# Performance work log

Measured on AMD Instinct MI355X. Metric: run time of the kernel, lower is better.

## Reference

```python
import jax, jax.numpy as jnp
import numpy as np

BN_EPS = 1e-5
LEAKY_SLOPE = 0.2


def setup_inputs() -> dict:
    key = jax.random.key(0)
    k1, k2 = jax.random.split(key, 2)
    B, C, N, O, K = 8, 64, 4096, 64, 20
    x = jax.random.normal(k1, (B, C, N), dtype=jnp.float32)
    W = jax.random.normal(k2, (O, 2 * C), dtype=jnp.float32) * 0.05  # 1x1 conv weight
    gamma = jnp.ones((O,), dtype=jnp.float32)
    beta = jnp.zeros((O,), dtype=jnp.float32)
    return {"x": x, "W": W, "gamma": gamma, "beta": beta, "k": K}


def reference(x, W, gamma, beta, k):
    # x: (B, C, N)
    xt = jnp.transpose(x, (0, 2, 1))  # (B, N, C)
    # kNN via squared euclidean distances (same ordering as cdist p=2)
    sq = jnp.sum(xt * xt, axis=-1)  # (B, N)
    d2 = sq[:, :, None] + sq[:, None, :] - 2.0 * jnp.einsum('bnc,bmc->bnm', xt, xt)
    idx = jax.lax.top_k(-d2, k)[1]  # (B, N, k) nearest neighbors (incl. self)
    # gather neighbor features: (B, N, k, C)
    xj = jax.vmap(lambda f, i: f[i])(xt, idx)
    xi = xt[:, :, None, :]  # (B, N, 1, C)
    edge = jnp.concatenate([xj - xi, jnp.broadcast_to(xi, xj.shape)], axis=-1)  # (B, N, k, 2C)
    # 1x1 conv == channel GEMM
    h = jnp.einsum('bnkc,oc->bnko', edge, W)  # (B, N, k, O)
    # BatchNorm2d, training-mode batch statistics over (B, N, k) per channel
    mean = jnp.mean(h, axis=(0, 1, 2))
    var = jnp.mean(jnp.square(h - mean), axis=(0, 1, 2))
    hn = (h - mean) * jax.lax.rsqrt(var + BN_EPS) * gamma + beta
    # LeakyReLU(0.2); dropout omitted (eval / identity)
    act = jnp.where(hn >= 0, hn, LEAKY_SLOPE * hn)
    # max over the k neighbors -> (B, N, O) -> (B, O, N)
    out = jnp.max(act, axis=2)
    return jnp.transpose(out, (0, 2, 1))
```

## Files before the change

kernel.cpp:

```cpp
#include <hip/hip_runtime.h>
#include <math.h>

#define Bn 8
#define Cc 64
#define Nn 4096
#define Oo 64
#define Kk 20
#define Kh 10
#define QCAP 24
#define NTOT (Bn*Nn*Kk)

typedef __attribute__((ext_vector_type(8))) short short8;
typedef __attribute__((ext_vector_type(4))) float f32x4;

__device__ __forceinline__ unsigned bf16_rn(float v) {
  unsigned u = __float_as_uint(v);
  return (u + 0x7FFFu + ((u >> 16) & 1)) >> 16;
}

__device__ __forceinline__ float pair_swap_f(float v) {
  return __int_as_float(__builtin_amdgcn_mov_dpp(__float_as_int(v), 0xB1, 0xF, 0xF, true));
}
__device__ __forceinline__ int pair_swap_i(int v) {
  return __builtin_amdgcn_mov_dpp(v, 0xB1, 0xF, 0xF, true);
}

__global__ __launch_bounds__(256) void k_split(const float* __restrict__ x,
                                               unsigned short* __restrict__ xs3,
                                               float* __restrict__ sqv) {
  __shared__ float xs[64][68];
  int tid = threadIdx.x;
  int b = blockIdx.x & 7;
  int n0 = (blockIdx.x >> 3) << 6;
  for (int i = 0; i < 4; i++) {
    int c = i * 16 + (tid >> 4);
    int n = (tid & 15) * 4;
    float4 v = *(const float4*)&x[((size_t)b * Cc + c) * Nn + n0 + n];
    *(float4*)&xs[c][n] = v;
  }
  __syncthreads();
  for (int i = 0; i < 4; i++) {
    int n = i * 16 + (tid >> 4);
    int c = (tid & 15) * 4;
    ushort4 h4, m4, l4;
    unsigned short* hp = (unsigned short*)&h4;
    unsigned short* mp = (unsigned short*)&m4;
    unsigned short* lp = (unsigned short*)&l4;
#pragma unroll
    for (int j = 0; j < 4; j++) {
      float v = xs[c + j][n];
      unsigned hb = bf16_rn(v);
      float hf = __uint_as_float(hb << 16);
      float r1 = v - hf;
      unsigned mb = bf16_rn(r1);
      float mf = __uint_as_float(mb << 16);
      float r2 = r1 - mf;
      unsigned lb = bf16_rn(r2);
      hp[j] = (unsigned short)hb;
      mp[j] = (unsigned short)mb;
      lp[j] = (unsigned short)lb;
    }
    size_t o = ((size_t)(b << 12) + n0 + n) * 192 + c;
    *(ushort4*)&xs3[o] = h4;
    *(ushort4*)&xs3[o + 64] = m4;
    *(ushort4*)&xs3[o + 128] = l4;
  }
  if (tid < 64) {
    float s = 0.f;
#pragma unroll
    for (int c = 0; c < 64; c++) { float v = xs[c][tid]; s = fmaf(v, v, s); }
    sqv[b * Nn + n0 + tid] = s;
  }
}

__global__ __launch_bounds__(256) void k_y1z(const float* __restrict__ x,
                                             const float* __restrict__ Wm,
                                             float* __restrict__ y1,
                                             float* __restrict__ z) {
  __shared__ float xs[64][68];
  __shared__ float Wl[64][129];
  int tid = threadIdx.x;
  int b = blockIdx.x & 7;
  int n0 = (blockIdx.x >> 3) << 6;
  for (int i = tid; i < 64 * 128; i += 256) Wl[i >> 7][i & 127] = Wm[i];
  for (int i = 0; i < 4; i++) {
    int c = i * 16 + (tid >> 4);
    int n = (tid & 15) * 4;
    float4 v = *(const float4*)&x[((size_t)b * Cc + c) * Nn + n0 + n];
    *(float4*)&xs[c][n] = v;
  }
  __syncthreads();
  int o = tid & 63, ng = tid >> 6;
  for (int p = 0; p < 4; p++) {
    int nb = p * 16 + ng * 4;
    float a1[4] = {0.f, 0.f, 0.f, 0.f};
    float a2[4] = {0.f, 0.f, 0.f, 0.f};
#pragma unroll 8
    for (int c = 0; c < 64; c++) {
      float4 xv = *(const float4*)&xs[c][nb];
      float w1v = Wl[o][c], w2v = Wl[o][64 + c];
      float xa[4] = {xv.x, xv.y, xv.z, xv.w};
#pragma unroll
      for (int j = 0; j < 4; j++) {
        a1[j] = fmaf(xa[j], w1v, a1[j]);
        a2[j] = fmaf(xa[j], w2v, a2[j]);
      }
    }
#pragma unroll
    for (int j = 0; j < 4; j++) {
      size_t off = ((size_t)b * Nn + n0 + nb + j) * 64 + o;
      y1[off] = a1[j];
      z[off] = a2[j] - a1[j];
    }
  }
}

__global__ __launch_bounds__(512, 4) void k_knn(const unsigned short* __restrict__ xs3,
                                                const float* __restrict__ sqv,
                                                int* __restrict__ idxout) {
  __shared__ alignas(16) short Bs[2][12288];
  __shared__ float thrS[2][64];
  __shared__ float sqs[2][64];
  __shared__ alignas(16) float qk[2][64][QCAP];
  __shared__ alignas(16) unsigned short qm[2][64][QCAP];
  __shared__ int qcnt[2][64];

  const int tid = threadIdx.x;
  const int lane = tid & 63;
  const int w = tid >> 6;
  const int grp = w >> 2;
  const int wg = w & 3;
  const int tig = tid & 255;
  const int b = blockIdx.x & 7;
  const int n0 = (blockIdx.x >> 3) << 6;
  const int lm = lane & 15;
  const int q = lane >> 4;
  const bool handler = (lane < 32);
  const int hrow = wg * 16 + (lane >> 1);
  const bool isL = (lane & 1) == 0;
  const int rowq = wg * 16 + q * 4;

  const unsigned long long fullseg = 0xFFFFull << (q * 16);
  const unsigned long long window = ((1ull << lane) - 1) & fullseg;

  float hk[Kh];
  int hix[Kh];
#pragma unroll
  for (int kk = 0; kk < Kh; kk++) { hk[kk] = INFINITY; hix[kk] = 0; }

  if (handler && !isL) { thrS[grp][hrow] = INFINITY; qcnt[grp][hrow] = 0; }

  const size_t arow = ((size_t)(b << 12) + n0 + wg * 16 + lm) * 192;
  short8 ah0 = *(const short8*)&xs3[arow + q * 8];
  short8 ah1 = *(const short8*)&xs3[arow + 32 + q * 8];
  short8 am0 = *(const short8*)&xs3[arow + 64 + q * 8];
  short8 am1 = *(const short8*)&xs3[arow + 96 + q * 8];
  short8 al0 = *(const short8*)&xs3[arow + 128 + q * 8];
  short8 al1 = *(const short8*)&xs3[arow + 160 + q * 8];

  const unsigned short* gp = xs3 + ((size_t)(b << 12) + grp * 2048) * 192 + tig * 8;
  short* ld[6];
#pragma unroll
  for (int i = 0; i < 6; i++) {
    int f = i * 256 + tig;
    int r = f / 24;
    ld[i] = &Bs[grp][(f * 8) ^ ((r & 7) << 3)];
  }
  const int qa = ((q ^ (lm & 7)) << 3);
  const int qb = (((q + 4) ^ (lm & 7)) << 3);
  const short* Bg = &Bs[grp][0];

  f32x4 acc[4];
  int qcr[4] = {0, 0, 0, 0};

  for (int t = 0; t < 32; t++) {
    const int m0 = grp * 2048 + t * 64;
    __syncthreads();
#pragma unroll
    for (int i = 0; i < 6; i++) {
      short8 v = *(const short8*)(gp + i * 2048);
      *(short8*)ld[i] = v;
    }
    gp += 12288;
    if (tig < 16) ((float4*)sqs[grp])[tig] = ((const float4*)(sqv + b * Nn + m0))[tig];
    __syncthreads();

#pragma unroll
    for (int g = 0; g < 4; g++) {
      const short* brow = Bg + (g * 16 + lm) * 192;
      short8 bh0 = *(const short8*)(brow + qa);
      short8 bh1 = *(const short8*)(brow + qb);
      short8 bm0 = *(const short8*)(brow + 64 + qa);
      short8 bm1 = *(const short8*)(brow + 64 + qb);
      short8 bl0 = *(const short8*)(brow + 128 + qa);
      short8 bl1 = *(const short8*)(brow + 128 + qb);
      f32x4 a = (f32x4){0.f, 0.f, 0.f, 0.f};
      a = __builtin_amdgcn_mfma_f32_16x16x32_bf16(am0, bm0, a, 0, 0, 0);
      a = __builtin_amdgcn_mfma_f32_16x16x32_bf16(am1, bm1, a, 0, 0, 0);
      a = __builtin_amdgcn_mfma_f32_16x16x32_bf16(ah0, bl0, a, 0, 0, 0);
      a = __builtin_amdgcn_mfma_f32_16x16x32_bf16(ah1, bl1, a, 0, 0, 0);
      a = __builtin_amdgcn_mfma_f32_16x16x32_bf16(al0, bh0, a, 0, 0, 0);
      a = __builtin_amdgcn_mfma_f32_16x16x32_bf16(al1, bh1, a, 0, 0, 0);
      a = __builtin_amdgcn_mfma_f32_16x16x32_bf16(ah0, bm0, a, 0, 0, 0);
      a = __builtin_amdgcn_mfma_f32_16x16x32_bf16(ah1, bm1, a, 0, 0, 0);
      a = __builtin_amdgcn_mfma_f32_16x16x32_bf16(am0, bh0, a, 0, 0, 0);
      a = __builtin_amdgcn_mfma_f32_16x16x32_bf16(am1, bh1, a, 0, 0, 0);
      a = __builtin_amdgcn_mfma_f32_16x16x32_bf16(ah0, bh0, a, 0, 0, 0);
      a = __builtin_amdgcn_mfma_f32_16x16x32_bf16(ah1, bh1, a, 0, 0, 0);
      acc[g] = a;
    }

    unsigned pend = 0;
    {
      float tl[4];
#pragma unroll
      for (int r = 0; r < 4; r++) tl[r] = thrS[grp][wg * 16 + q * 4 + r];
      if (grp) {
#pragma unroll
        for (int r = 0; r < 4; r++) tl[r] = fminf(tl[r], thrS[0][wg * 16 + q * 4 + r]);
      }
#pragma unroll
      for (int g = 0; g < 4; g++) {
        float sv = sqs[grp][g * 16 + lm];
#pragma unroll
        for (int r = 0; r < 4; r++) {
          float key = fmaf(-2.f, acc[g][r], sv);
          acc[g][r] = key;
          if (key < tl[r]) pend |= 1u << (g * 4 + r);
        }
      }
    }

    for (;;) {
      unsigned long long havep = __ballot(pend != 0);
      if (havep) {
#pragma unroll
        for (int g = 0; g < 4; g++) {
#pragma unroll
          for (int r = 0; r < 4; r++) {
            const unsigned bit = 1u << (g * 4 + r);
            bool want = (pend & bit) != 0;
            unsigned long long mask = __ballot(want);
            int cnt = (int)__builtin_popcountll(mask & fullseg);
            int off = (int)__builtin_popcountll(mask & window);
            int p = qcr[r] + off;
            if (want && p < QCAP) {
              qk[grp][rowq + r][p] = acc[g][r];
              qm[grp][rowq + r][p] = (unsigned short)(m0 + g * 16 + lm);
              pend &= ~bit;
            }
            int nq = qcr[r] + cnt;
            qcr[r] = nq > QCAP ? QCAP : nq;
          }
        }
        if (lm == 0) {
          qcnt[grp][rowq + 0] = qcr[0];
          qcnt[grp][rowq + 1] = qcr[1];
          qcnt[grp][rowq + 2] = qcr[2];
          qcnt[grp][rowq + 3] = qcr[3];
        }
      }
      unsigned long long anyovf = __ballot(pend != 0);

      if (handler) {
        int cn = qcnt[grp][hrow];
        for (int p0 = 0; p0 < cn; p0 += 2) {
          float2 kv2 = *(const float2*)&qk[grp][hrow][p0];
          ushort2 mv2 = *(const ushort2*)&qm[grp][hrow][p0];
          float kva[2] = {kv2.x, kv2.y};
          unsigned short mva[2] = {mv2.x, mv2.y};
#pragma unroll
          for (int j = 0; j < 2; j++) {
            bool valid = (p0 + j < cn);
            float kv = kva[j];
            int ki = (int)mva[j];
            bool lins = kv < hk[Kh - 1];
            float pv_ = lins ? hk[Kh - 1] : kv;
            int pi_ = lins ? hix[Kh - 1] : ki;
            float rv = pair_swap_f(pv_);
            int ri = pair_swap_i(pi_);
            float mval = isL ? kv : rv;
            int midx = isL ? ki : ri;
            if (valid && mval < hk[Kh - 1]) {
              bool cm[Kh];
#pragma unroll
              for (int kk = 0; kk < Kh; kk++) cm[kk] = mval < hk[kk];
#pragma unroll
              for (int kk = Kh - 1; kk >= 1; kk--) {
                hk[kk]  = cm[kk] ? (cm[kk - 1] ? hk[kk - 1]  : mval) : hk[kk];
                hix[kk] = cm[kk] ? (cm[kk - 1] ? hix[kk - 1] : midx) : hix[kk];
              }
              if (cm[0]) { hk[0] = mval; hix[0] = midx; }
            }
          }
        }
        if (cn && !isL) { qcnt[grp][hrow] = 0; thrS[grp][hrow] = hk[Kh - 1]; }
      }
      qcr[0] = 0; qcr[1] = 0; qcr[2] = 0; qcr[3] = 0;
      if (!anyovf) break;
      if (pend) {
        float tl[4];
#pragma unroll
        for (int r = 0; r < 4; r++) tl[r] = thrS[grp][wg * 16 + q * 4 + r];
        if (grp) {
#pragma unroll
          for (int r = 0; r < 4; r++) tl[r] = fminf(tl[r], thrS[0][wg * 16 + q * 4 + r]);
        }
#pragma unroll
        for (int g = 0; g < 4; g++)
#pragma unroll
          for (int r = 0; r < 4; r++) {
            unsigned bit = 1u << (g * 4 + r);
            if ((pend & bit) && acc[g][r] >= tl[r]) pend &= ~bit;
          }
      }
    }
  }

  if (grp == 1 && handler) {
    int base = isL ? 0 : Kh;
#pragma unroll
    for (int kk = 0; kk < Kh; kk++) {
      qk[1][hrow][base + kk] = hk[kk];
      qm[1][hrow][base + kk] = (unsigned short)hix[kk];
    }
  }
  __syncthreads();
  if (grp == 0 && handler) {
    for (int p0 = 0; p0 < Kk; p0 += 4) {
      float4 kv4 = *(const float4*)&qk[1][hrow][p0];
      ushort4 mv4 = *(const ushort4*)&qm[1][hrow][p0];
      float kva[4] = {kv4.x, kv4.y, kv4.z, kv4.w};
      unsigned short mva[4] = {mv4.x, mv4.y, mv4.z, mv4.w};
#pragma unroll
    for (int j = 0; j < 4; j++) {
        float kv = kva[j];
        int ki = (int)mva[j];
        bool lins = kv < hk[Kh - 1];
        float pv_ = lins ? hk[Kh - 1] : kv;
        int pi_ = lins ? hix[Kh - 1] : ki;
        float rv = pair_swap_f(pv_);
        int ri = pair_swap_i(pi_);
        float mval = isL ? kv : rv;
        int midx = isL ? ki : ri;
        if (mval < hk[Kh - 1]) {
          bool cm[Kh];
#pragma unroll
          for (int kk = 0; kk < Kh; kk++) cm[kk] = mval < hk[kk];
#pragma unroll
          for (int kk = Kh - 1; kk >= 1; kk--) {
            hk[kk]  = cm[kk] ? (cm[kk - 1] ? hk[kk - 1]  : mval) : hk[kk];
            hix[kk] = cm[kk] ? (cm[kk - 1] ? hix[kk - 1] : midx) : hix[kk];
          }
          if (cm[0]) { hk[0] = mval; hix[0] = midx; }
        }
      }
    }
    size_t obase = ((size_t)b * Nn + n0 + hrow) * Kk + (isL ? 0 : Kh);
#pragma unroll
    for (int kk = 0; kk < Kh; kk++) idxout[obase + kk] = hix[kk];
  }
}

__global__ __launch_bounds__(256) void k_stats(const float* __restrict__ y1,
                                               const float* __restrict__ z,
                                               const int* __restrict__ idxp,
                                               float* __restrict__ parts) {
  __shared__ float rs[4][64];
  __shared__ float rq[4][64];
  int tid = threadIdx.x;
  int o = tid & 63, g = tid >> 6;
  int b = blockIdx.x & 7;
  int n0 = (blockIdx.x >> 3) << 6;
  const float* y1b = y1 + (size_t)b * Nn * 64;
  float s = 0.f, ss = 0.f;
  for (int t = 0; t < 16; t++) {
    int n = n0 + g + t * 4;
    size_t base = (size_t)b * Nn + n;
    float zv = z[base * 64 + o];
    const int* ip = idxp + base * Kk;
#pragma unroll
    for (int k = 0; k < Kk; k++) {
      int j = ip[k];
      float hv = y1b[(size_t)j * 64 + o] + zv;
      s += hv;
      ss = fmaf(hv, hv, ss);
    }
  }
  rs[g][o] = s;
  rq[g][o] = ss;
  __syncthreads();
  if (tid < 64) {
    parts[(size_t)blockIdx.x * 128 + tid] = rs[0][tid] + rs[1][tid] + rs[2][tid] + rs[3][tid];
    parts[(size_t)blockIdx.x * 128 + 64 + tid] = rq[0][tid] + rq[1][tid] + rq[2][tid] + rq[3][tid];
  }
}

__global__ __launch_bounds__(128) void k_reduce(const float* __restrict__ parts,
                                                float* __restrict__ stats) {
  int tid = threadIdx.x;
  float s = 0.f;
  for (int i = 0; i < 512; i += 4) {
    s += parts[(size_t)i * 128 + tid] + parts[(size_t)(i + 1) * 128 + tid] +
         parts[(size_t)(i + 2) * 128 + tid] + parts[(size_t)(i + 3) * 128 + tid];
  }
  stats[tid] = s;
}

__global__ __launch_bounds__(256) void k_out(const float* __restrict__ y1,
                                             const float* __restrict__ z,
                                             const int* __restrict__ idxp,
                                             const float* __restrict__ stats,
                                             const float* __restrict__ gamma,
                                             const float* __restrict__ beta,
                                             float* __restrict__ out) {
  __shared__ float T[64][65];
  int tid = threadIdx.x;
  int lane = tid & 63;
  int w = tid >> 6;
  int b = blockIdx.x & 7;
  int n0 = (blockIdx.x >> 3) << 6;
  int o = lane;
  const float inv = 1.0f / (float)NTOT;
  float mean = stats[o] * inv;
  float var = fmaf(-mean, mean, stats[64 + o] * inv);
  float sc = gamma[o] * rsqrtf(var + 1e-5f);
  float bi = fmaf(-mean, sc, beta[o]);
  const float* y1b = y1 + (size_t)b * Nn * 64;
  for (int t = 0; t < 16; t++) {
    int nl = w + t * 4;
    size_t base = (size_t)b * Nn + n0 + nl;
    float zv = z[base * 64 + o];
    const int* ip = idxp + base * Kk;
    float mv = -INFINITY;
#pragma unroll
    for (int k = 0; k < Kk; k++) {
      int j = ip[k];
      float hv = y1b[(size_t)j * 64 + o] + zv;
      float hn = fmaf(hv, sc, bi);
      float a = (hn >= 0.f) ? hn : 0.2f * hn;
      mv = fmaxf(mv, a);
    }
    T[o][nl] = mv;
  }
  __syncthreads();
  for (int t = 0; t < 16; t++) {
    int oo = w * 16 + t;
    out[((size_t)b * Oo + oo) * Nn + n0 + lane] = T[oo][lane];
  }
}

extern "C" void kernel_launch(void* const* d_in, const int* in_sizes, int n_in,
                              void* d_out, int out_size, void* d_ws, size_t ws_size,
                              hipStream_t stream) {
  const float* x = (const float*)d_in[0];
  const float* W = (const float*)d_in[1];
  const float* gamma = (const float*)d_in[2];
  const float* beta = (const float*)d_in[3];

  char* ws = (char*)d_ws;
  unsigned short* xs3 = (unsigned short*)ws;
  float* y1 = (float*)ws;
  float* z = (float*)(ws + 8388608);
  float* sq = (float*)(ws + 16777216);
  float* stats = (float*)(ws + 16908288);
  int* idx = (int*)(ws + 16908800);
  float* parts = (float*)(ws + 19530240);
  float* out = (float*)d_out;

  k_split<<<Bn * (Nn / 64), 256, 0, stream>>>(x, xs3, sq);
  k_knn<<<Bn * (Nn / 64), 512, 0, stream>>>(xs3, sq, idx);
  k_y1z<<<Bn * (Nn / 64), 256, 0, stream>>>(x, W, y1, z);
  k_stats<<<Bn * (Nn / 64), 256, 0, stream>>>(y1, z, idx, parts);
  k_reduce<<<1, 128, 0, stream>>>(parts, stats);
  k_out<<<Bn * (Nn / 64), 256, 0, stream>>>(y1, z, idx, stats, gamma, beta, out);
}
```

Before: 398.3 us.

## Use direct global-to-LDS loads and LDS atomics for kNN candidate queueing

Tile loads of the bf16-split point features and the squared norms now go straight from global memory into LDS through global_load_lds, so they no longer pass through registers. The swizzle moves to the global source address so the LDS layout stays the same. Candidate enqueueing switches from per-(g,r) wave ballots with popcount offsets to per-row LDS atomicAdd on qcnt, and the handler clamps the count to QCAP. Threshold reads become float4 loads. The atomics can serialize on hot rows, and the direct-to-LDS path depends on the 64-lane contiguous destination addressing being correct.

```diff
diff --git a/kernel.cpp b/kernel.cpp
--- a/kernel.cpp
+++ b/kernel.cpp
@@ -23,6 +23,12 @@
 }
 __device__ __forceinline__ int pair_swap_i(int v) {
   return __builtin_amdgcn_mov_dpp(v, 0xB1, 0xF, 0xF, true);
+}
+
+__device__ __forceinline__ void gload_lds16(const void* g, void* l) {
+  __builtin_amdgcn_global_load_lds((const __attribute__((address_space(1))) void*)g,
+                                   (__attribute__((address_space(3))) void*)l,
+                                   16, 0, 0);
 }
 
 __global__ __launch_bounds__(256) void k_split(const float* __restrict__ x,
@@ -119,8 +125,8 @@
                                                 const float* __restrict__ sqv,
                                                 int* __restrict__ idxout) {
   __shared__ alignas(16) short Bs[2][12288];
-  __shared__ float thrS[2][64];
-  __shared__ float sqs[2][64];
+  __shared__ alignas(16) float thrS[2][64];
+  __shared__ alignas(16) float sqs[2][64];
   __shared__ alignas(16) float qk[2][64][QCAP];
   __shared__ alignas(16) unsigned short qm[2][64][QCAP];
   __shared__ int qcnt[2][64];
@@ -140,9 +146,6 @@
   const bool isL = (lane & 1) == 0;
   const int rowq = wg * 16 + q * 4;
 
-  const unsigned long long fullseg = 0xFFFFull << (q * 16);
-  const unsigned long long window = ((1ull << lane) - 1) & fullseg;
-
   float hk[Kh];
   int hix[Kh];
 #pragma unroll
@@ -158,31 +161,29 @@
   short8 al0 = *(const short8*)&xs3[arow + 128 + q * 8];
   short8 al1 = *(const short8*)&xs3[arow + 160 + q * 8];
 
-  const unsigned short* gp = xs3 + ((size_t)(b << 12) + grp * 2048) * 192 + tig * 8;
-  short* ld[6];
+  const unsigned short* gbase = xs3 + ((size_t)(b << 12) + grp * 2048) * 192;
+  int gofs[6];
+  short* lbase[6];
 #pragma unroll
   for (int i = 0; i < 6; i++) {
-    int f = i * 256 + tig;
-    int r = f / 24;
-    ld[i] = &Bs[grp][(f * 8) ^ ((r & 7) << 3)];
+    int p = i * 256 + wg * 64 + lane;
+    int gsrc = p ^ ((p / 24) & 7);
+    gofs[i] = gsrc * 8;
+    lbase[i] = &Bs[grp][(i * 256 + wg * 64) * 8];
   }
   const int qa = ((q ^ (lm & 7)) << 3);
   const int qb = (((q + 4) ^ (lm & 7)) << 3);
   const short* Bg = &Bs[grp][0];
 
   f32x4 acc[4];
-  int qcr[4] = {0, 0, 0, 0};
 
   for (int t = 0; t < 32; t++) {
     const int m0 = grp * 2048 + t * 64;
     __syncthreads();
 #pragma unroll
-    for (int i = 0; i < 6; i++) {
-      short8 v = *(const short8*)(gp + i * 2048);
-      *(short8*)ld[i] = v;
-    }
-    gp += 12288;
-    if (tig < 16) ((float4*)sqs[grp])[tig] = ((const float4*)(sqv + b * Nn + m0))[tig];
+    for (int i = 0; i < 6; i++) gload_lds16(gbase + gofs[i], lbase[i]);
+    if (tig < 16) gload_lds16(sqv + b * Nn + m0 + lane * 4, &sqs[grp][0]);
+    gbase += 12288;
     __syncthreads();
 
 #pragma unroll
@@ -212,12 +213,12 @@
 
     unsigned pend = 0;
     {
-      float tl[4];
-#pragma unroll
-      for (int r = 0; r < 4; r++) tl[r] = thrS[grp][wg * 16 + q * 4 + r];
+      float4 t4 = *(const float4*)&thrS[grp][rowq];
+      float tl[4] = {t4.x, t4.y, t4.z, t4.w};
       if (grp) {
-#pragma unroll
-        for (int r = 0; r < 4; r++) tl[r] = fminf(tl[r], thrS[0][wg * 16 + q * 4 + r]);
+        float4 s4 = *(const float4*)&thrS[0][rowq];
+        tl[0] = fminf(tl[0], s4.x); tl[1] = fminf(tl[1], s4.y);
+        tl[2] = fminf(tl[2], s4.z); tl[3] = fminf(tl[3], s4.w);
       }
 #pragma unroll
       for (int g = 0; g < 4; g++) {
@@ -232,38 +233,29 @@
     }
 
     for (;;) {
-      unsigned long long havep = __ballot(pend != 0);
-      if (havep) {
+      if (pend) {
 #pragma unroll
         for (int g = 0; g < 4; g++) {
 #pragma unroll
           for (int r = 0; r < 4; r++) {
-            const unsigned bit = 1u << (g * 4 + r);
-            bool want = (pend & bit) != 0;
-            unsigned long long mask = __ballot(want);
-            int cnt = (int)__builtin_popcountll(mask & fullseg);
-            int off = (int)__builtin_popcountll(mask & window);
-            int p = qcr[r] + off;
-            if (want && p < QCAP) {
-              qk[grp][rowq + r][p] = acc[g][r];
-              qm[grp][rowq + r][p] = (unsigned short)(m0 + g * 16 + lm);
-              pend &= ~bit;
+            unsigned bit = 1u << (g * 4 + r);
+            if (pend & bit) {
+              int row = rowq + r;
+              int p = atomicAdd(&qcnt[grp][row], 1);
+              if (p < QCAP) {
+                qk[grp][row][p] = acc[g][r];
+                qm[grp][row][p] = (unsigned short)(m0 + g * 16 + lm);
+                pend &= ~bit;
+              }
             }
-            int nq = qcr[r] + cnt;
-            qcr[r] = nq > QCAP ? QCAP : nq;
           }
         }
-        if (lm == 0) {
-          qcnt[grp][rowq + 0] = qcr[0];
-          qcnt[grp][rowq + 1] = qcr[1];
-          qcnt[grp][rowq + 2] = qcr[2];
-          qcnt[grp][rowq + 3] = qcr[3];
-        }
       }
       unsigned long long anyovf = __ballot(pend != 0);
 
       if (handler) {
         int cn = qcnt[grp][hrow];
+        if (cn > QCAP) cn = QCAP;
         for (int p0 = 0; p0 < cn; p0 += 2) {
           float2 kv2 = *(const float2*)&qk[grp][hrow][p0];
           ushort2 mv2 = *(const ushort2*)&qm[grp][hrow][p0];
@@ -296,15 +288,14 @@
         }
         if (cn && !isL) { qcnt[grp][hrow] = 0; thrS[grp][hrow] = hk[Kh - 1]; }
       }
-      qcr[0] = 0; qcr[1] = 0; qcr[2] = 0; qcr[3] = 0;
       if (!anyovf) break;
       if (pend) {
-        float tl[4];
-#pragma unroll
-        for (int r = 0; r < 4; r++) tl[r] = thrS[grp][wg * 16 + q * 4 + r];
+        float4 t4 = *(const float4*)&thrS[grp][rowq];
+        float tl[4] = {t4.x, t4.y, t4.z, t4.w};
         if (grp) {
-#pragma unroll
-          for (int r = 0; r < 4; r++) tl[r] = fminf(tl[r], thrS[0][wg * 16 + q * 4 + r]);
+          float4 s4 = *(const float4*)&thrS[0][rowq];
+          tl[0] = fminf(tl[0], s4.x); tl[1] = fminf(tl[1], s4.y);
+          tl[2] = fminf(tl[2], s4.z); tl[3] = fminf(tl[3], s4.w);
         }
 #pragma unroll
         for (int g = 0; g < 4; g++)
@@ -333,7 +324,7 @@
       float kva[4] = {kv4.x, kv4.y, kv4.z, kv4.w};
       unsigned short mva[4] = {mv4.x, mv4.y, mv4.z, mv4.w};
 #pragma unroll
-    for (int j = 0; j < 4; j++) {
+      for (int j = 0; j < 4; j++) {
         float kv = kva[j];
         int ki = (int)mva[j];
         bool lins = kv < hk[Kh - 1];
```

Result: faster. 364.9 us (-8.4%).
